# Kernel tuning notes

Measured on AMD Instinct MI355X. Metric: run time of the kernel, lower is better.

The kernel has to match this reference:

```python
import jax, jax.numpy as jnp
import numpy as np


def _run_lstm(x, W, U, b, mask=None):
    """Keras-style LSTM returning final hidden state.
    x: [N, T, D] float; W: [D, 4u]; U: [u, 4u]; b: [4u]; mask: [N, T] bool or None.
    Gate order i, f, g(c), o as in Keras. Masked steps carry state through.
    """
    N, T, D = x.shape
    units = U.shape[0]
    xt = jnp.transpose(x, (1, 0, 2))  # [T, N, D]
    if mask is not None:
        mt = jnp.transpose(mask, (1, 0))[:, :, None]  # [T, N, 1]
        xs = (xt, mt)
    else:
        xs = xt

    def step(carry, inp):
        h, c = carry
        if mask is not None:
            x_t, m = inp
        else:
            x_t = inp
        z = x_t @ W + h @ U + b  # [N, 4u]
        i, f, g, o = jnp.split(z, 4, axis=-1)
        i = jax.nn.sigmoid(i)
        f = jax.nn.sigmoid(f)
        g = jnp.tanh(g)
        o = jax.nn.sigmoid(o)
        c_new = f * c + i * g
        h_new = o * jnp.tanh(c_new)
        if mask is not None:
            h_new = jnp.where(m, h_new, h)
            c_new = jnp.where(m, c_new, c)
        return (h_new, c_new), None

    h0 = jnp.zeros((N, units), dtype=x.dtype)
    c0 = jnp.zeros((N, units), dtype=x.dtype)
    (hT, _), _ = jax.lax.scan(step, (h0, c0), xs)
    return hT


def setup_inputs() -> dict:
    key = jax.random.key(0)
    ks = jax.random.split(key, 10)
    B, T, S, D = 256, 256, 20, 1
    U1, U2 = 32, 24  # inner / outer LSTM units
    sc = 0.1
    x = jax.random.normal(ks[0], (B, T, S, D), dtype=jnp.float32)
    lengths = jax.random.randint(ks[1], (B,), 1, T + 1, dtype=jnp.int32)
    Wi = jax.random.normal(ks[2], (D, 4 * U1), dtype=jnp.float32) * sc
    Ui = jax.random.normal(ks[3], (U1, 4 * U1), dtype=jnp.float32) * sc
    bi = jnp.zeros((4 * U1,), dtype=jnp.float32)
    Wo = jax.random.normal(ks[4], (U1, 4 * U2), dtype=jnp.float32) * sc
    Uo = jax.random.normal(ks[5], (U2, 4 * U2), dtype=jnp.float32) * sc
    bo = jnp.zeros((4 * U2,), dtype=jnp.float32)
    Wd = jax.random.normal(ks[6], (U2, 1), dtype=jnp.float32) * sc
    bd = jnp.zeros((1,), dtype=jnp.float32)
    return {"x": x, "lengths": lengths, "Wi": Wi, "Ui": Ui, "bi": bi,
            "Wo": Wo, "Uo": Uo, "bo": bo, "Wd": Wd, "bd": bd}


def reference(x, lengths, Wi, Ui, bi, Wo, Uo, bo, Wd, bd):
    B, T, S, D = x.shape
    # TimeDistributed(LSTM(32)): run inner LSTM over each outer step (inference, dropout off)
    rows = x.reshape(B * T, S, D)
    h_inner = _run_lstm(rows, Wi, Ui, bi)          # [B*T, 32]
    feats = h_inner.reshape(B, T, -1)              # [B, T, 32]
    # Outer LSTM(24) with ragged-length mask (Keras mask semantics: carry state)
    mask = jnp.arange(T)[None, :] < lengths[:, None]  # [B, T]
    h_outer = _run_lstm(feats, Wo, Uo, bo, mask)   # [B, 24]
    # Dense sigmoid head
    return jax.nn.sigmoid(h_outer @ Wd + bd)       # [B, 1]
```

## Files before the change

kernel.cpp:

```cpp
#include <hip/hip_runtime.h>

#define B_  256
#define T_  256
#define S_  20
#define U1  32
#define G1  128
#define U2  24
#define G2  96
#define NT  16

typedef __attribute__((ext_vector_type(8))) short short8;
typedef __attribute__((ext_vector_type(4))) float f32x4;
typedef __attribute__((ext_vector_type(2))) float f32x2;

#define KSIG  (-1.44269504f)
#define KTANH ( 2.88539008f)

__device__ __forceinline__ float sigmoidf_(float x) {
    return __builtin_amdgcn_rcpf(1.0f + __builtin_amdgcn_exp2f(x * KSIG));
}
__device__ __forceinline__ float tanhf_fast(float x) {
    return 1.0f - 2.0f * __builtin_amdgcn_rcpf(1.0f + __builtin_amdgcn_exp2f(x * KTANH));
}
__device__ __forceinline__ float dpp_xor1(float x) {
    return __int_as_float(__builtin_amdgcn_update_dpp(
        0, __float_as_int(x), 0xB1, 0xF, 0xF, true));
}
__device__ __forceinline__ f32x2 dexp2(f32x2 z, float k) {
    f32x2 t = z * k;
    f32x2 e;
    e.x = __builtin_amdgcn_exp2f(t.x);
    e.y = __builtin_amdgcn_exp2f(t.y);
    return e + 1.0f;
}
__device__ __forceinline__ void brcp4(f32x2 d01, f32x2 d23, f32x2& s01, f32x2& s23) {
    const f32x2 m = d01 * d23;
    f32x2 R;
    R.x = __builtin_amdgcn_rcpf(m.x);
    R.y = __builtin_amdgcn_rcpf(m.y);
    s01 = R * d23;
    s23 = R * d01;
}

__device__ __forceinline__ unsigned short f2bf(float a) {
    unsigned int u = __float_as_uint(a);
    u += 0x7FFFu + ((u >> 16) & 1u);
    return (unsigned short)(u >> 16);
}
__device__ __forceinline__ unsigned int pack2bf(float a, float b) {
    unsigned int ua = __float_as_uint(a); ua += 0x7FFFu + ((ua >> 16) & 1u);
    unsigned int ub = __float_as_uint(b); ub += 0x7FFFu + ((ub >> 16) & 1u);
    return (ua >> 16) | (ub & 0xFFFF0000u);
}
union frag_u { short8 v; unsigned int u[4]; };
union h2x  { unsigned int u32; _Float16 h[2]; };

__global__ __attribute__((amdgpu_flat_work_group_size(512, 512)))
__attribute__((amdgpu_waves_per_eu(2, 2)))
void fused_kernel(
    const float* __restrict__ x,
    const int*   __restrict__ lengths,
    const float* __restrict__ Wi,
    const float* __restrict__ Ui,
    const float* __restrict__ bi,
    const float* __restrict__ Wo,
    const float* __restrict__ Uo,
    const float* __restrict__ bo,
    const float* __restrict__ Wd,
    const float* __restrict__ bd,
    float* __restrict__ out)
{
    __shared__ __align__(16) _Float16      Pl[T_][G2];
    __shared__ __align__(16) unsigned short hbb[8][16][40];
    __shared__ unsigned int flags[NT];
    const int b    = blockIdx.x;
    const int len  = lengths[b];
    const int tid  = threadIdx.x;
    const int w    = __builtin_amdgcn_readfirstlane(tid >> 6);
    const int lane = tid & 63;
    const int q    = lane >> 4;
    const int n    = lane & 15;

    if (tid < NT) flags[tid] = 0;
    __syncthreads();

    if (w <= 3) __builtin_amdgcn_s_setprio(2);

    frag_u Bui[8];
#pragma unroll
    for (int tt = 0; tt < 8; ++tt)
#pragma unroll
        for (int k2 = 0; k2 < 4; ++k2)
            Bui[tt].u[k2] = pack2bf(Ui[(8 * q + 2 * k2) * G1 + 16 * tt + n],
                                    Ui[(8 * q + 2 * k2 + 1) * G1 + 16 * tt + n]);
    frag_u Bwo[6];
#pragma unroll
    for (int tt = 0; tt < 6; ++tt)
#pragma unroll
        for (int k2 = 0; k2 < 4; ++k2)
            Bwo[tt].u[k2] = pack2bf(Wo[(8 * q + 2 * k2) * G2 + 16 * tt + n],
                                    Wo[(8 * q + 2 * k2 + 1) * G2 + 16 * tt + n]);
    float bi_l[8], Wi_l[8], bo_l[6];
#pragma unroll
    for (int tt = 0; tt < 8; ++tt) { bi_l[tt] = bi[16 * tt + n]; Wi_l[tt] = Wi[16 * tt + n]; }
#pragma unroll
    for (int tt = 0; tt < 6; ++tt) bo_l[tt] = bo[16 * tt + n];
    int pcol[6];
#pragma unroll
    for (int tt = 0; tt < 6; ++tt) {
        const int col = 16 * tt + n;
        const int g = col / 24;
        pcol[tt] = (col - 24 * g) * 4 + g;
    }

    int tl[3]; int ntl;
    if (w == 0)      { tl[0] = 0; tl[1] = 0; tl[2] = 0; ntl = 1; }
    else if (w == 1) { tl[0] = 1; tl[1] = 8; tl[2] = 9; ntl = 3; }
    else             { tl[0] = w; tl[1] = w + 8; tl[2] = 0; ntl = 2; }

#pragma unroll 1
    for (int i = 0; i < ntl; ++i) {
        const int tile = tl[i];
        const int wt0  = tile * 16;
        if (wt0 >= len) break;

        const float* xr = x + (size_t)(b * T_ + wt0 + 4 * q) * S_;
        f32x2 c01[2], c23[2];
#pragma unroll
        for (int uh = 0; uh < 2; ++uh) { c01[uh] = {0.0f, 0.0f}; c23[uh] = {0.0f, 0.0f}; }

        auto activate = [&](f32x4* acc) {
#pragma unroll
            for (int uh = 0; uh < 2; ++uh) {
                const f32x2 zi01 = { acc[0 + uh][0], acc[0 + uh][1] };
                const f32x2 zi23 = { acc[0 + uh][2], acc[0 + uh][3] };
                const f32x2 zf01 = { acc[2 + uh][0], acc[2 + uh][1] };
                const f32x2 zf23 = { acc[2 + uh][2], acc[2 + uh][3] };
                const f32x2 zg01 = { acc[4 + uh][0], acc[4 + uh][1] };
                const f32x2 zg23 = { acc[4 + uh][2], acc[4 + uh][3] };
                const f32x2 zo01 = { acc[6 + uh][0], acc[6 + uh][1] };
                const f32x2 zo23 = { acc[6 + uh][2], acc[6 + uh][3] };

                f32x2 si01, si23, sf01, sf23, rg01, rg23, so01, so23;
                brcp4(dexp2(zi01, KSIG),  dexp2(zi23, KSIG),  si01, si23);
                brcp4(dexp2(zf01, KSIG),  dexp2(zf23, KSIG),  sf01, sf23);
                brcp4(dexp2(zg01, KTANH), dexp2(zg23, KTANH), rg01, rg23);
                brcp4(dexp2(zo01, KSIG),  dexp2(zo23, KSIG),  so01, so23);
                const f32x2 g01 = 1.0f - 2.0f * rg01;
                const f32x2 g23 = 1.0f - 2.0f * rg23;
                c01[uh] = sf01 * c01[uh] + si01 * g01;
                c23[uh] = sf23 * c23[uh] + si23 * g23;
                f32x2 rc01, rc23;
                brcp4(dexp2(c01[uh], KTANH), dexp2(c23[uh], KTANH), rc01, rc23);
                const f32x2 t01 = 1.0f - 2.0f * rc01;
                const f32x2 t23 = 1.0f - 2.0f * rc23;
                const f32x2 h01 = so01 * t01;
                const f32x2 h23 = so23 * t23;
                hbb[w][4 * q + 0][n + 16 * uh] = f2bf(h01.x);
                hbb[w][4 * q + 1][n + 16 * uh] = f2bf(h01.y);
                hbb[w][4 * q + 2][n + 16 * uh] = f2bf(h23.x);
                hbb[w][4 * q + 3][n + 16 * uh] = f2bf(h23.y);
            }
        };

        float xc[4];
#pragma unroll
        for (int r = 0; r < 4; ++r) xc[r] = xr[r * S_];

        {
            f32x4 acc[8];
#pragma unroll
            for (int tt = 0; tt < 8; ++tt)
#pragma unroll
                for (int r = 0; r < 4; ++r)
                    acc[tt][r] = bi_l[tt] + xc[r] * Wi_l[tt];
            activate(acc);
        }
#pragma unroll
        for (int r = 0; r < 4; ++r) xc[r] = xr[r * S_ + 1];

#pragma unroll 1
        for (int s = 1; s < S_; ++s) {
            const int sn = (s + 1 < S_) ? s + 1 : S_ - 1;
            float xnx[4];
#pragma unroll
            for (int r = 0; r < 4; ++r) xnx[r] = xr[r * S_ + sn];

            f32x4 acc[8];
#pragma unroll
            for (int tt = 0; tt < 8; ++tt)
#pragma unroll
                for (int r = 0; r < 4; ++r)
                    acc[tt][r] = bi_l[tt] + xc[r] * Wi_l[tt];

            const short8 A = *(const short8*)&hbb[w][n][8 * q];
#pragma unroll
            for (int tt = 0; tt < 8; ++tt)
                acc[tt] = __builtin_amdgcn_mfma_f32_16x16x32_bf16(A, Bui[tt].v, acc[tt], 0, 0, 0);

            activate(acc);
#pragma unroll
            for (int r = 0; r < 4; ++r) xc[r] = xnx[r];
        }

        {
            const short8 A = *(const short8*)&hbb[w][n][8 * q];
            f32x4 accp[6];
#pragma unroll
            for (int tt = 0; tt < 6; ++tt) {
#pragma unroll
                for (int r = 0; r < 4; ++r) accp[tt][r] = bo_l[tt];
                accp[tt] = __builtin_amdgcn_mfma_f32_16x16x32_bf16(A, Bwo[tt].v, accp[tt], 0, 0, 0);
            }
#pragma unroll
            for (int r = 0; r < 4; ++r) {
                const int tr = wt0 + 4 * q + r;
#pragma unroll
                for (int tt = 0; tt < 6; ++tt)
                    Pl[tr][pcol[tt]] = (_Float16)accp[tt][r];
            }
        }
        __hip_atomic_store(&flags[tile], 1u, __ATOMIC_RELEASE, __HIP_MEMORY_SCOPE_WORKGROUP);
        if (i == 0) {
            if (w == 0) __builtin_amdgcn_s_setprio(1);
            else        __builtin_amdgcn_s_setprio(0);
        }
    }

    if (w != 0) return;

    const int p = lane & 1;
    const int u = (lane < 2 * U2) ? (lane >> 1) : (U2 - 1);
    const int cA = p ? (2 * U2 + u) : u;
    const int cB = p ? (3 * U2 + u) : (U2 + u);

    const f32x2 kAB = { p ? KTANH : KSIG, KSIG };
    const f32x2 mAB = { p ? -2.0f : 1.0f, 1.0f };
    const f32x2 aAB = { p ?  1.0f : 0.0f, 0.0f };

    auto gates2 = [&](f32x2 z) -> f32x2 {
        const f32x2 t = z * kAB;
        f32x2 e;
        e.x = __builtin_amdgcn_exp2f(t.x);
        e.y = __builtin_amdgcn_exp2f(t.y);
        const f32x2 d = e + 1.0f;
        f32x2 r;
        r.x = __builtin_amdgcn_rcpf(d.x);
        r.y = __builtin_amdgcn_rcpf(d.y);
        return r * mAB + aAB;
    };

    f32x2 w2_[U2];
#pragma unroll
    for (int k = 0; k < U2; ++k) {
        w2_[k].x = Uo[k * G2 + cA];
        w2_[k].y = Uo[k * G2 + cB];
    }

    auto ldrow2 = [&](int t) -> f32x2 {
        const uint2 raw = *reinterpret_cast<const uint2*>(&Pl[t][4 * u]);
        h2x s_; s_.u32 = p ? raw.y : raw.x;
        f32x2 r; r.x = (float)s_.h[0]; r.y = (float)s_.h[1];
        return r;
    };

    float cu = 0.0f, hu;
    {
        const f32x2 out2 = gates2(ldrow2(0));
        const float tg  = dpp_xor1(out2.x);
        cu = out2.x * tg;
        const float tc  = tanhf_fast(cu);
        const float tcs = dpp_xor1(tc);
        hu = out2.y * tcs;
    }
    int wtile = 0;
    f32x2 nxt = ldrow2((1 < len) ? 1 : 0);

#pragma unroll 1
    for (int t = 1; t < len; ++t) {
        const int tn = (t + 1 < len) ? (t + 1) : (len - 1);
        const int ttile = tn >> 4;
        if (ttile != wtile) {
            while (__hip_atomic_load(&flags[ttile], __ATOMIC_ACQUIRE,
                                     __HIP_MEMORY_SCOPE_WORKGROUP) == 0u)
                __builtin_amdgcn_s_sleep(1);
            wtile = ttile;
        }
        const f32x2 pf = ldrow2(tn);

        float hk[U2];
#pragma unroll
        for (int k = 0; k < U2; ++k)
            hk[k] = __int_as_float(__builtin_amdgcn_readlane(__float_as_int(hu), 2 * k + 1));

        f32x2 ab0 = nxt;
        f32x2 ab1 = {0.0f, 0.0f}, ab2 = {0.0f, 0.0f}, ab3 = {0.0f, 0.0f};
#pragma unroll
        for (int k = 0; k < U2; k += 4) {
            ab0 += w2_[k]     * hk[k];
            ab1 += w2_[k + 1] * hk[k + 1];
            ab2 += w2_[k + 2] * hk[k + 2];
            ab3 += w2_[k + 3] * hk[k + 3];
        }
        const f32x2 zz = (ab0 + ab1) + (ab2 + ab3);

        const f32x2 out2 = gates2(zz);
        const float tg  = dpp_xor1(out2.x);
        cu = out2.y * cu + out2.x * tg;
        const float tc  = tanhf_fast(cu);
        const float tcs = dpp_xor1(tc);
        hu = out2.y * tcs;

        nxt = pf;
    }

    float acc = bd[0];
#pragma unroll
    for (int k = 0; k < U2; ++k)
        acc += __int_as_float(__builtin_amdgcn_readlane(__float_as_int(hu), 2 * k + 1)) * Wd[k];
    if (lane == 0) out[b] = sigmoidf_(acc);
}

extern "C" void kernel_launch(void* const* d_in, const int* in_sizes, int n_in,
                              void* d_out, int out_size, void* d_ws, size_t ws_size,
                              hipStream_t stream) {
    const float* x       = (const float*)d_in[0];
    const int*   lengths = (const int*)  d_in[1];
    const float* Wi      = (const float*)d_in[2];
    const float* Ui      = (const float*)d_in[3];
    const float* bi      = (const float*)d_in[4];
    const float* Wo      = (const float*)d_in[5];
    const float* Uo      = (const float*)d_in[6];
    const float* bo      = (const float*)d_in[7];
    const float* Wd      = (const float*)d_in[8];
    const float* bd      = (const float*)d_in[9];
    float* out = (float*)d_out;

    fused_kernel<<<dim3(B_), dim3(512), 0, stream>>>(
        x, lengths, Wi, Ui, bi, Wo, Uo, bo, Wd, bd, out);
}
```

Measured before the change: 149.4 us.

## Batch-prefetch outer-LSTM projection tiles into register double buffers

The outer LSTM recurrence now loads a whole 16-step tile of precomputed input projections from LDS into registers, double-buffered, instead of loading one row per step. The flag wait and loads for the next tile are issued mid-tile, and the inner loop is fully unrolled per tile. This takes per-step LDS loads, tile-boundary checks and flag polling off the serial recurrence critical path. In exchange it uses more registers (two 16-entry buffers) and much larger unrolled code, and it relies on goto-based early exit for ragged lengths.

```diff
diff --git a/kernel.cpp b/kernel.cpp
--- a/kernel.cpp
+++ b/kernel.cpp
@@ -257,68 +257,93 @@
         w2_[k].y = Uo[k * G2 + cB];
     }
 
-    auto ldrow2 = [&](int t) -> f32x2 {
-        const uint2 raw = *reinterpret_cast<const uint2*>(&Pl[t][4 * u]);
-        h2x s_; s_.u32 = p ? raw.y : raw.x;
-        f32x2 r; r.x = (float)s_.h[0]; r.y = (float)s_.h[1];
-        return r;
-    };
-
-    float cu = 0.0f, hu;
+    const int rowoff = 8 * u + 4 * p;
+    const char* Pb = reinterpret_cast<const char*>(&Pl[0][0]);
+    const int ntiles = (len + 15) >> 4;
+
+    unsigned bufA[16], bufB[16];
+
+    float cu = 0.0f, hu = 0.0f;
+
+#define STEP_ROW(RW) do {                                                     \
+    h2x s_; s_.u32 = (RW);                                                    \
+    f32x2 pr; pr.x = (float)s_.h[0]; pr.y = (float)s_.h[1];                   \
+    float hk[U2];                                                             \
+    _Pragma("unroll")                                                         \
+    for (int kq = 0; kq < U2; ++kq)                                           \
+        hk[kq] = __int_as_float(                                              \
+            __builtin_amdgcn_readlane(__float_as_int(hu), 2 * kq + 1));       \
+    f32x2 ab0 = pr;                                                           \
+    f32x2 ab1 = {0.0f, 0.0f}, ab2 = {0.0f, 0.0f}, ab3 = {0.0f, 0.0f};         \
+    _Pragma("unroll")                                                         \
+    for (int kq = 0; kq < U2; kq += 4) {                                      \
+        ab0 += w2_[kq]     * hk[kq];                                          \
+        ab1 += w2_[kq + 1] * hk[kq + 1];                                      \
+        ab2 += w2_[kq + 2] * hk[kq + 2];                                      \
+        ab3 += w2_[kq + 3] * hk[kq + 3];                                      \
+    }                                                                         \
+    const f32x2 zz = (ab0 + ab1) + (ab2 + ab3);                               \
+    const f32x2 o2 = gates2(zz);                                              \
+    const float tg  = dpp_xor1(o2.x);                                         \
+    cu = o2.y * cu + o2.x * tg;                                               \
+    const float tc  = tanhf_fast(cu);                                         \
+    const float tcs = dpp_xor1(tc);                                           \
+    hu = o2.y * tcs;                                                          \
+} while (0)
+
+#define TILE_BODY(K, CUR, NXT, J0) do {                                       \
+    _Pragma("unroll")                                                         \
+    for (int j = (J0); j < 8; ++j) {                                          \
+        if (16 * (K) + j >= len) goto p2done;                                 \
+        STEP_ROW(CUR[j]);                                                     \
+    }                                                                         \
+    if ((K) + 1 < ntiles) {                                                   \
+        while (__hip_atomic_load(&flags[(K) + 1], __ATOMIC_ACQUIRE,           \
+                                 __HIP_MEMORY_SCOPE_WORKGROUP) == 0u)         \
+            __builtin_amdgcn_s_sleep(1);                                      \
+        _Pragma("unroll")                                                     \
+        for (int j = 0; j < 16; ++j)                                          \
+            NXT[j] = *reinterpret_cast<const unsigned*>(                      \
+                Pb + (16 * ((K) + 1) + j) * (G2 * 2) + rowoff);               \
+    }                                                                         \
+    _Pragma("unroll")                                                         \
+    for (int j = 8; j < 16; ++j) {                                            \
+        if (16 * (K) + j >= len) goto p2done;                                 \
+        STEP_ROW(CUR[j]);                                                     \
+    }                                                                         \
+} while (0)
+
+#pragma unroll
+    for (int j = 0; j < 16; ++j)
+        bufA[j] = *reinterpret_cast<const unsigned*>(Pb + j * (G2 * 2) + rowoff);
+
     {
-        const f32x2 out2 = gates2(ldrow2(0));
-        const float tg  = dpp_xor1(out2.x);
-        cu = out2.x * tg;
+        h2x s_; s_.u32 = bufA[0];
+        f32x2 z0; z0.x = (float)s_.h[0]; z0.y = (float)s_.h[1];
+        const f32x2 o2 = gates2(z0);
+        const float tg  = dpp_xor1(o2.x);
+        cu = o2.x * tg;
         const float tc  = tanhf_fast(cu);
         const float tcs = dpp_xor1(tc);
-        hu = out2.y * tcs;
-    }
-    int wtile = 0;
-    f32x2 nxt = ldrow2((1 < len) ? 1 : 0);
-
+        hu = o2.y * tcs;
+    }
+
+    TILE_BODY(0, bufA, bufB, 1);
 #pragma unroll 1
-    for (int t = 1; t < len; ++t) {
-        const int tn = (t + 1 < len) ? (t + 1) : (len - 1);
-        const int ttile = tn >> 4;
-        if (ttile != wtile) {
-            while (__hip_atomic_load(&flags[ttile], __ATOMIC_ACQUIRE,
-                                     __HIP_MEMORY_SCOPE_WORKGROUP) == 0u)
-                __builtin_amdgcn_s_sleep(1);
-            wtile = ttile;
-        }
-        const f32x2 pf = ldrow2(tn);
-
-        float hk[U2];
-#pragma unroll
-        for (int k = 0; k < U2; ++k)
-            hk[k] = __int_as_float(__builtin_amdgcn_readlane(__float_as_int(hu), 2 * k + 1));
-
-        f32x2 ab0 = nxt;
-        f32x2 ab1 = {0.0f, 0.0f}, ab2 = {0.0f, 0.0f}, ab3 = {0.0f, 0.0f};
-#pragma unroll
-        for (int k = 0; k < U2; k += 4) {
-            ab0 += w2_[k]     * hk[k];
-            ab1 += w2_[k + 1] * hk[k + 1];
-            ab2 += w2_[k + 2] * hk[k + 2];
-            ab3 += w2_[k + 3] * hk[k + 3];
-        }
-        const f32x2 zz = (ab0 + ab1) + (ab2 + ab3);
-
-        const f32x2 out2 = gates2(zz);
-        const float tg  = dpp_xor1(out2.x);
-        cu = out2.y * cu + out2.x * tg;
-        const float tc  = tanhf_fast(cu);
-        const float tcs = dpp_xor1(tc);
-        hu = out2.y * tcs;
-
-        nxt = pf;
-    }
+    for (int k = 1; k < ntiles; ++k) {
+        if (k & 1) TILE_BODY(k, bufB, bufA, 0);
+        else       TILE_BODY(k, bufA, bufB, 0);
+    }
+p2done: ;
 
     float acc = bd[0];
 #pragma unroll
     for (int k = 0; k < U2; ++k)
         acc += __int_as_float(__builtin_amdgcn_readlane(__float_as_int(hu), 2 * k + 1)) * Wd[k];
     if (lane == 0) out[b] = sigmoidf_(acc);
+
+#undef TILE_BODY
+#undef STEP_ROW
 }
 
 extern "C" void kernel_launch(void* const* d_in, const int* in_sizes, int n_in,
```

Measured after the change: 149.3 us. About the same (-0.0%).
